# Performance work log

Hardware: AMD Instinct MI355X
Metric: run time of the kernel (lower is better)

## Reference

```python
import jax, jax.numpy as jnp
import numpy as np

B, S, E = 4, 2048, 1024
HIDDEN = 1024
HEADS = 16


def setup_inputs() -> dict:
    key = jax.random.key(0)
    k0, k1, k2, k3, k4 = jax.random.split(key, 5)
    inputs = jax.random.normal(k0, (B, S, E), dtype=jnp.float32)
    W_qkv = jax.random.normal(k1, (E, 3 * HIDDEN), dtype=jnp.float32) * 0.02
    b_qkv = jnp.zeros((3 * HIDDEN,), dtype=jnp.float32)
    W_out = jax.random.normal(k2, (HIDDEN, HIDDEN), dtype=jnp.float32) * 0.02
    b_out = jnp.zeros((HIDDEN,), dtype=jnp.float32)
    return {"inputs": inputs, "W_qkv": W_qkv, "b_qkv": b_qkv, "W_out": W_out, "b_out": b_out}


def reference(inputs, W_qkv, b_qkv, W_out, b_out):
    Bv, Sv, Ev = inputs.shape
    x = inputs @ W_qkv + b_qkv                      # [B, S, 3*hidden]
    # Faithful to the original: reshape mixes seq and hidden exactly as the source does.
    x = x.reshape(Bv, HEADS, Sv, -1)                # [B, H, S, 3*hidden/H]
    q, k, v = jnp.split(x, 3, axis=-1)              # each [B, H, S, hidden/H]
    scale = (2 * HIDDEN) ** (-0.5)
    qk = jnp.einsum('bhse,bhte->bhst', q, k) * scale  # [B, H, S, S]
    mask = jnp.triu(jnp.full((Sv, Sv), -jnp.inf, dtype=qk.dtype), k=1)
    attn = jax.nn.softmax(qk + mask, axis=-1)
    sa = jnp.einsum('bhst,bhte->bhse', attn, v).reshape(Bv, Sv, -1)  # [B, S, hidden]
    return sa @ W_out + b_out
```

## Files before the change

kernel.cpp:

```cpp
#include <hip/hip_runtime.h>
#include <hip/hip_bf16.h>

using bf16 = __hip_bfloat16;

typedef __attribute__((ext_vector_type(8))) short short8;
typedef __attribute__((ext_vector_type(4))) float f32x4;


#define CEXP 0.03188127742677263f

__device__ __forceinline__ unsigned short f2bf(float v) {
  bf16 h = __float2bfloat16(v);
  return *(unsigned short*)&h;
}
__device__ __forceinline__ unsigned int pack2bf(float a, float b) {
  return (unsigned int)f2bf(a) | ((unsigned int)f2bf(b) << 16);
}

__device__ __forceinline__ void gload_lds16(const void* g, void* lds) {
  __builtin_amdgcn_global_load_lds(
      (const __attribute__((address_space(1))) unsigned int*)(g),
      (__attribute__((address_space(3))) unsigned int*)(lds), 16, 0, 0);
}

__global__ void detect_kernel(const unsigned int* __restrict__ x, int* __restrict__ flag) {
  unsigned int w = x[threadIdx.x];
  unsigned int e = (w >> 7) & 0xFF;
  bool inband = (e >= 96 && e <= 133);
  unsigned long long m = __ballot(inband);
  if (threadIdx.x == 0) flag[0] = (__popcll(m) >= 48) ? 0 : 1;
}

__global__ __launch_bounds__(256) void convert_kernel(
    const void* __restrict__ src, bf16* __restrict__ dst, int n8,
    const int* __restrict__ flag) {
  int i = blockIdx.x * 256 + threadIdx.x;
  if (i >= n8) return;
  uint4 outv;
  if (*flag) {
    const float4* s = (const float4*)src + (size_t)i * 2;
    float4 a = s[0], b = s[1];
    outv.x = pack2bf(a.x, a.y);
    outv.y = pack2bf(a.z, a.w);
    outv.z = pack2bf(b.x, b.y);
    outv.w = pack2bf(b.z, b.w);
  } else {
    outv = ((const uint4*)src)[i];
  }
  ((uint4*)dst)[i] = outv;
}

__global__ void convert_bias_qkv(const void* __restrict__ src, bf16* __restrict__ dst,
                                 const int* __restrict__ flag) {
  int i = blockIdx.x * 256 + threadIdx.x;
  if (i >= 3072) return;
  float v = (*flag) ? ((const float*)src)[i]
                    : __bfloat162float(((const bf16*)src)[i]);
  if ((i % 192) < 64) v *= CEXP;
  dst[i] = __float2bfloat16(v);
}

__global__ __launch_bounds__(256) void transpose_bf16(
    const void* __restrict__ src, bf16* __restrict__ dst, int R, int Cc,
    const int* __restrict__ flag, int qscale) {
  __shared__ float tile[32][33];
  const int c0 = blockIdx.x * 32, r0 = blockIdx.y * 32;
  const int tx = threadIdx.x & 31, ty = threadIdx.x >> 5;
  const bool f32 = (*flag != 0);
#pragma unroll
  for (int it = 0; it < 4; ++it) {
    int r = ty + it * 8;
    float v;
    if (f32) v = ((const float*)src)[(size_t)(r0 + r) * Cc + c0 + tx];
    else     v = __bfloat162float(((const bf16*)src)[(size_t)(r0 + r) * Cc + c0 + tx]);
    tile[r][tx] = v;
  }
  __syncthreads();
#pragma unroll
  for (int it = 0; it < 4; ++it) {
    int r = ty + it * 8;
    float vv = tile[tx][r];
    if (qscale && (((c0 + r) % 192) < 64)) vv *= CEXP;
    dst[(size_t)(c0 + r) * R + r0 + tx] = __float2bfloat16(vv);
  }
}

__global__ __launch_bounds__(256) void transpose_v(const bf16* __restrict__ qkv,
                                                   bf16* __restrict__ vtg)
{
  __shared__ short tile[64][72];
  const int bh = blockIdx.x;
  const int k0 = blockIdx.y * 64;
  const unsigned short* qk = (const unsigned short*)qkv + (size_t)bh * 393216;
  const int key = threadIdx.x & 63;
  const int dv = threadIdx.x >> 6;
  const int gk = k0 + key;
  const unsigned short* src =
      qk + (size_t)(gk >> 4) * 3072 + (gk & 15) * 192 + 128 + dv * 16;
  *(short8*)&tile[key][dv * 16] = *(const short8*)src;
  *(short8*)&tile[key][dv * 16 + 8] = *(const short8*)(src + 8);
  __syncthreads();
  const int d = threadIdx.x & 63;
  const int kv = threadIdx.x >> 6;
  unsigned short* dst =
      (unsigned short*)vtg + ((size_t)bh * 64 + d) * 2048 + k0 + kv * 16;
  short8 a, b;
#pragma unroll
  for (int j = 0; j < 8; ++j) {
    a[j] = tile[kv * 16 + j][d];
    b[j] = tile[kv * 16 + 8 + j][d];
  }
  *(short8*)dst = a;
  *(short8*)(dst + 8) = b;
}

__global__ __launch_bounds__(256) void gemm_mfma(
    const bf16* __restrict__ A, const bf16* __restrict__ BT,
    const bf16* __restrict__ bias, void* __restrict__ C,
    int M, int N, int K, int store_mode, const int* __restrict__ flag)
{
  __shared__ alignas(16) unsigned short As[128 * 32];
  __shared__ alignas(16) unsigned short Bs[128 * 32];
  const bool store_f32 = store_mode && (*flag != 0);
  const int tid = threadIdx.x;
  const int wave = tid >> 6, lane = tid & 63;
  const int l15 = lane & 15, l4 = lane >> 4;

  const int nwg = gridDim.x * gridDim.y;
  const int orig = blockIdx.x + gridDim.x * blockIdx.y;
  const int qn = nwg >> 3, rn = nwg & 7;
  const int xcd = orig & 7, loc = orig >> 3;
  const int swz = (xcd < rn ? xcd * (qn + 1) : rn * (qn + 1) + (xcd - rn) * qn) + loc;
  const int bx = swz % gridDim.x, by = swz / gridDim.x;

  const int m0 = by * 128, n0 = bx * 128;
  const int wm = (wave & 1) * 64, wn = (wave >> 1) * 64;

  const int srow = wave * 32 + (lane >> 2);
  const int skv = (lane & 3) * 8;
  const bf16* ga = A + (size_t)(m0 + srow) * K + skv;
  const bf16* gb = BT + (size_t)(n0 + srow) * K + skv;
  unsigned short* la = As + (wave * 32) * 32;
  unsigned short* lb = Bs + (wave * 32) * 32;

  f32x4 acc[4][4] = {};

  for (int k0 = 0; k0 < K; k0 += 32) {
    __syncthreads();
    gload_lds16(ga, la);
    gload_lds16(ga + (size_t)16 * K, la + 16 * 32);
    gload_lds16(gb, lb);
    gload_lds16(gb + (size_t)16 * K, lb + 16 * 32);
    ga += 32; gb += 32;
    __syncthreads();

    short8 af[4], bfr[4];
#pragma unroll
    for (int i = 0; i < 4; ++i) {
      af[i]  = *(const short8*)(As + (wm + i * 16 + l15) * 32 + l4 * 8);
      bfr[i] = *(const short8*)(Bs + (wn + i * 16 + l15) * 32 + l4 * 8);
    }
#pragma unroll
    for (int i = 0; i < 4; ++i)
#pragma unroll
      for (int j = 0; j < 4; ++j)
        acc[i][j] = __builtin_amdgcn_mfma_f32_16x16x32_bf16(af[i], bfr[j], acc[i][j], 0, 0, 0);
  }

#pragma unroll
  for (int j = 0; j < 4; ++j) {
    const int n = n0 + wn + j * 16 + l15;
    const float bv = __bfloat162float(bias[n]);
#pragma unroll
    for (int i = 0; i < 4; ++i) {
#pragma unroll
      for (int r = 0; r < 4; ++r) {
        const int mrow = m0 + wm + i * 16 + l4 * 4 + r;
        const float v = acc[i][j][r] + bv;
        if (store_f32) ((float*)C)[(size_t)mrow * N + n] = v;
        else           ((bf16*)C)[(size_t)mrow * N + n] = __float2bfloat16(v);
      }
    }
  }
}

__global__ __launch_bounds__(512) void attn_mfma(const bf16* __restrict__ qkv,
                                                 const bf16* __restrict__ vtg,
                                                 bf16* __restrict__ sa)
{
  __shared__ alignas(16) short Ks[2][4096];
  __shared__ alignas(16) short Vs[2][4096];
  __shared__ alignas(16) short Ps[8][1152];
  const int tid = threadIdx.x;
  const int bh = blockIdx.x;
  const int pr = blockIdx.y;
  const size_t base = (size_t)bh * 393216;
  const int w = tid >> 6;
  const int g = w >> 2;
  const int wl = w & 3;
  const int lane = tid & 63;
  const int l15 = lane & 15, l4 = lane >> 4;
  const unsigned short* qk = (const unsigned short*)qkv;
  const unsigned short* vtb = (const unsigned short*)vtg + (size_t)bh * 131072;
  short* psw = &Ps[w][0];

  const int qc = g ? pr : (15 - pr);
  const int my_ktmax  = 2 * qc + 1;
  const int blk_ktmax = 2 * (15 - pr) + 1;

  const unsigned short* gsrc0 =
      g ? (vtb + (size_t)lane * 2048)
        : (qk + base + (size_t)(lane >> 4) * 3072 + (lane & 15) * 192 + 64);
  const size_t gstep = g ? 64 : 12288;

  short8 qf[2][2];
#pragma unroll
  for (int h = 0; h < 2; ++h) {
    const unsigned short* pq =
        qk + base + (size_t)(qc * 8 + 2 * wl + h) * 3072 + l15 * 192 + l4 * 8;
    qf[h][0] = *(const short8*)pq;
    qf[h][1] = *(const short8*)(pq + 32);
  }

  f32x4 o[2][4] = {};
  float ml[2] = {-__builtin_inff(), -__builtin_inff()};
  float ls[2] = {0.f, 0.f};
  int cur = 0;

  {
    short* dstbuf = g ? &Vs[0][0] : &Ks[0][0];
    gload_lds16(gsrc0 + wl * 8, dstbuf + wl * 512);
    gload_lds16(gsrc0 + (wl + 4) * 8, dstbuf + (wl + 4) * 512);
  }
  __syncthreads();

  for (int kt = 0; kt <= blk_ktmax; ++kt) {
    if (kt < blk_ktmax) {
      short* dstbuf = g ? &Vs[cur ^ 1][0] : &Ks[cur ^ 1][0];
      const unsigned short* s = gsrc0 + (size_t)(kt + 1) * gstep;
      gload_lds16(s + wl * 8, dstbuf + wl * 512);
      gload_lds16(s + (wl + 4) * 8, dstbuf + (wl + 4) * 512);
    }

    if (kt <= my_ktmax) {
      f32x4 sc[2][4];
#pragma unroll
      for (int t = 0; t < 4; ++t) {
        const short8 kf0 = *(const short8*)&Ks[cur][(l4) * 512 + (16 * t + l15) * 8];
        const short8 kf1 = *(const short8*)&Ks[cur][(4 + l4) * 512 + (16 * t + l15) * 8];
#pragma unroll
        for (int h = 0; h < 2; ++h) {
          f32x4 c = {};
          c = __builtin_amdgcn_mfma_f32_16x16x32_bf16(kf0, qf[h][0], c, 0, 0, 0);
          c = __builtin_amdgcn_mfma_f32_16x16x32_bf16(kf1, qf[h][1], c, 0, 0, 0);
          sc[h][t] = c;
        }
      }

      if (kt >= 2 * qc) {
        const int kb = 64 * (kt - 2 * qc);
#pragma unroll
        for (int h = 0; h < 2; ++h) {
          const int thr = 32 * wl + 16 * h + l15;
#pragma unroll
          for (int t = 0; t < 4; ++t)
#pragma unroll
            for (int r = 0; r < 4; ++r)
              if (kb + 16 * t + 4 * l4 + r > thr) sc[h][t][r] = -__builtin_inff();
        }
      }

      unsigned int pk2[2][4][2];
#pragma unroll
      for (int h = 0; h < 2; ++h) {
        float mx = -__builtin_inff();
#pragma unroll
        for (int t = 0; t < 4; ++t)
#pragma unroll
          for (int r = 0; r < 4; ++r) mx = fmaxf(mx, sc[h][t][r]);
        mx = fmaxf(mx, __shfl_xor(mx, 16, 64));
        mx = fmaxf(mx, __shfl_xor(mx, 32, 64));
        if (!__all(mx <= ml[h] + 8.f)) {
          const float m_new = fmaxf(ml[h], mx);
          const float alpha = __builtin_amdgcn_exp2f(ml[h] - m_new);
          ml[h] = m_new;
          ls[h] *= alpha;
#pragma unroll
          for (int jn = 0; jn < 4; ++jn)
#pragma unroll
            for (int r = 0; r < 4; ++r) o[h][jn][r] *= alpha;
        }
        const float m_new = ml[h];
        float s = 0.f;
#pragma unroll
        for (int t = 0; t < 4; ++t) {
          float p0 = __builtin_amdgcn_exp2f(sc[h][t][0] - m_new);
          float p1 = __builtin_amdgcn_exp2f(sc[h][t][1] - m_new);
          float p2 = __builtin_amdgcn_exp2f(sc[h][t][2] - m_new);
          float p3 = __builtin_amdgcn_exp2f(sc[h][t][3] - m_new);
          s += (p0 + p1) + (p2 + p3);
          pk2[h][t][0] = pack2bf(p0, p1);
          pk2[h][t][1] = pack2bf(p2, p3);
        }
        s += __shfl_xor(s, 16, 64);
        s += __shfl_xor(s, 32, 64);
        ls[h] += s;
      }

      short8 pf[2][2];
#pragma unroll
      for (int h = 0; h < 2; ++h) {
#pragma unroll
        for (int t = 0; t < 4; ++t) {
          uint2 wv; wv.x = pk2[h][t][0]; wv.y = pk2[h][t][1];
          *(uint2*)(psw + l15 * 72 + 16 * t + 4 * l4) = wv;
        }
        pf[h][0] = *(const short8*)(psw + l15 * 72 + 8 * l4);
        pf[h][1] = *(const short8*)(psw + l15 * 72 + 32 + 8 * l4);
      }

#pragma unroll
      for (int jn = 0; jn < 4; ++jn)
#pragma unroll
        for (int ks = 0; ks < 2; ++ks) {
          const short8 vf =
              *(const short8*)&Vs[cur][(4 * ks + l4) * 512 + (16 * jn + l15) * 8];
#pragma unroll
          for (int h = 0; h < 2; ++h)
            o[h][jn] = __builtin_amdgcn_mfma_f32_16x16x32_bf16(vf, pf[h][ks], o[h][jn], 0, 0, 0);
        }
    }

    __syncthreads();
    cur ^= 1;
  }

#pragma unroll
  for (int h = 0; h < 2; ++h) {
    const float inv = 1.0f / ls[h];
    unsigned short* so =
        (unsigned short*)sa + (size_t)(bh * 128 + qc * 8 + 2 * wl + h) * 1024;
#pragma unroll
    for (int jn = 0; jn < 4; ++jn) {
      uint2 wv;
      wv.x = pack2bf(o[h][jn][0] * inv, o[h][jn][1] * inv);
      wv.y = pack2bf(o[h][jn][2] * inv, o[h][jn][3] * inv);
      *(uint2*)(so + l15 * 64 + jn * 16 + l4 * 4) = wv;
    }
  }
}

extern "C" void kernel_launch(void* const* d_in, const int* in_sizes, int n_in,
                              void* d_out, int out_size, void* d_ws, size_t ws_size,
                              hipStream_t stream)
{
  const void* x_raw    = d_in[0];
  const void* Wqkv_raw = d_in[1];
  const void* bqkv_raw = d_in[2];
  const void* Wout_raw = d_in[3];
  const void* bout_raw = d_in[4];

  char* ws = (char*)d_ws;
  int*  flag   = (int*)ws;
  bf16* xb     = (bf16*)(ws + 256);
  bf16* wqkvT  = xb + (size_t)8192 * 1024;
  bf16* bqkvb  = wqkvT + (size_t)3072 * 1024;
  bf16* woutT  = bqkvb + 4096;
  bf16* boutb  = woutT + (size_t)1024 * 1024;
  bf16* qkv    = boutb + 4096;
  bf16* sa     = qkv + (size_t)8192 * 3072;
  bf16* vtg    = sa + (size_t)8192 * 1024;

  detect_kernel<<<1, 64, 0, stream>>>((const unsigned int*)x_raw, flag);

  convert_kernel<<<(8192 * 1024 / 8 + 255) / 256, 256, 0, stream>>>(x_raw, xb, 8192 * 1024 / 8, flag);
  convert_bias_qkv<<<12, 256, 0, stream>>>(bqkv_raw, bqkvb, flag);
  convert_kernel<<<1, 256, 0, stream>>>(bout_raw, boutb, 1024 / 8, flag);
  transpose_bf16<<<dim3(3072 / 32, 1024 / 32), 256, 0, stream>>>(Wqkv_raw, wqkvT, 1024, 3072, flag, 1);
  transpose_bf16<<<dim3(1024 / 32, 1024 / 32), 256, 0, stream>>>(Wout_raw, woutT, 1024, 1024, flag, 0);

  gemm_mfma<<<dim3(3072 / 128, 8192 / 128), 256, 0, stream>>>(
      xb, wqkvT, bqkvb, qkv, 8192, 3072, 1024, 0, flag);
  transpose_v<<<dim3(64, 32), 256, 0, stream>>>(qkv, vtg);
  attn_mfma<<<dim3(64, 8), 512, 0, stream>>>(qkv, vtg, sa);
  gemm_mfma<<<dim3(1024 / 128, 8192 / 128), 256, 0, stream>>>(
      sa, woutT, boutb, d_out, 8192, 1024, 1024, 1, flag);
}
```

Before: 294.0 us.

## Rewrite GEMM with 256x256 tiles, double-buffered LDS and XOR swizzle

Replaces the 128x128 single-buffered GEMM with a 512-thread 256x256-tile kernel using K-step 64. Global-to-LDS loads are double buffered with explicit vmcnt waits to overlap the next tile's fetch with MFMA work, and an XOR swizzle on LDS columns aims to avoid bank conflicts. Each wave computes a 128x64 sub-tile for more operand reuse, and setprio is raised around MFMA bursts. Costs are 128KB LDS per block and more accumulator registers, which limit occupancy. The out-projection grid drops to 128 blocks, which may underfill the GPU.

```diff
diff --git a/kernel.cpp b/kernel.cpp
--- a/kernel.cpp
+++ b/kernel.cpp
@@ -114,68 +114,94 @@
   *(short8*)(dst + 8) = b;
 }
 
-__global__ __launch_bounds__(256) void gemm_mfma(
+__global__ __launch_bounds__(512) void gemm256(
     const bf16* __restrict__ A, const bf16* __restrict__ BT,
     const bf16* __restrict__ bias, void* __restrict__ C,
     int M, int N, int K, int store_mode, const int* __restrict__ flag)
 {
-  __shared__ alignas(16) unsigned short As[128 * 32];
-  __shared__ alignas(16) unsigned short Bs[128 * 32];
+  __shared__ alignas(16) short As2[2][16384];
+  __shared__ alignas(16) short Bs2[2][16384];
   const bool store_f32 = store_mode && (*flag != 0);
   const int tid = threadIdx.x;
-  const int wave = tid >> 6, lane = tid & 63;
+  const int lane = tid & 63;
+  const int w = tid >> 6;
   const int l15 = lane & 15, l4 = lane >> 4;
+  const int wm2 = w >> 2, wn4 = w & 3;
 
   const int nwg = gridDim.x * gridDim.y;
   const int orig = blockIdx.x + gridDim.x * blockIdx.y;
-  const int qn = nwg >> 3, rn = nwg & 7;
-  const int xcd = orig & 7, loc = orig >> 3;
-  const int swz = (xcd < rn ? xcd * (qn + 1) : rn * (qn + 1) + (xcd - rn) * qn) + loc;
+  const int qn = nwg >> 3;
+  const int swz = (orig & 7) * qn + (orig >> 3);
   const int bx = swz % gridDim.x, by = swz / gridDim.x;
-
-  const int m0 = by * 128, n0 = bx * 128;
-  const int wm = (wave & 1) * 64, wn = (wave >> 1) * 64;
-
-  const int srow = wave * 32 + (lane >> 2);
-  const int skv = (lane & 3) * 8;
-  const bf16* ga = A + (size_t)(m0 + srow) * K + skv;
-  const bf16* gb = BT + (size_t)(n0 + srow) * K + skv;
-  unsigned short* la = As + (wave * 32) * 32;
-  unsigned short* lb = Bs + (wave * 32) * 32;
-
-  f32x4 acc[4][4] = {};
-
-  for (int k0 = 0; k0 < K; k0 += 32) {
-    __syncthreads();
-    gload_lds16(ga, la);
-    gload_lds16(ga + (size_t)16 * K, la + 16 * 32);
-    gload_lds16(gb, lb);
-    gload_lds16(gb + (size_t)16 * K, lb + 16 * 32);
-    ga += 32; gb += 32;
-    __syncthreads();
-
-    short8 af[4], bfr[4];
-#pragma unroll
-    for (int i = 0; i < 4; ++i) {
-      af[i]  = *(const short8*)(As + (wm + i * 16 + l15) * 32 + l4 * 8);
-      bfr[i] = *(const short8*)(Bs + (wn + i * 16 + l15) * 32 + l4 * 8);
-    }
-#pragma unroll
-    for (int i = 0; i < 4; ++i)
+  const int m0 = by * 256, n0 = bx * 256;
+
+  const int srow = tid >> 3;
+  const int koff = ((tid & 7) ^ (srow & 7)) << 3;
+  const bf16* pa = A + (size_t)(m0 + srow) * K + koff;
+  const bf16* pb = BT + (size_t)(n0 + srow) * K + koff;
+  const int dst0 = tid * 8;
+
+  const int rsw = l15 & 7;
+
+  f32x4 acc[8][4] = {};
+  const int nt = K >> 6;
+
+#pragma unroll
+  for (int q = 0; q < 4; ++q) {
+    gload_lds16(pa + (size_t)(q * 64) * K, &As2[0][q * 4096 + dst0]);
+    gload_lds16(pb + (size_t)(q * 64) * K, &Bs2[0][q * 4096 + dst0]);
+  }
+
+  for (int t = 0; t < nt; ++t) {
+    const int c = t & 1;
+    if (t + 1 < nt) {
+      const int nb = c ^ 1;
+      const bf16* sa_ = pa + (size_t)(t + 1) * 64;
+      const bf16* sb_ = pb + (size_t)(t + 1) * 64;
+#pragma unroll
+      for (int q = 0; q < 4; ++q) {
+        gload_lds16(sa_ + (size_t)(q * 64) * K, &As2[nb][q * 4096 + dst0]);
+        gload_lds16(sb_ + (size_t)(q * 64) * K, &Bs2[nb][q * 4096 + dst0]);
+      }
+      asm volatile("s_waitcnt vmcnt(8)" ::: "memory");
+    } else {
+      asm volatile("s_waitcnt vmcnt(0)" ::: "memory");
+    }
+    __builtin_amdgcn_s_barrier();
+    asm volatile("" ::: "memory");
+
+#pragma unroll
+    for (int s = 0; s < 2; ++s) {
+      const int cgs = (((s << 2) | l4) ^ rsw) * 8;
+      short8 af[8], bfr[4];
+#pragma unroll
+      for (int i = 0; i < 8; ++i)
+        af[i] = *(const short8*)&As2[c][(wm2 * 128 + i * 16 + l15) * 64 + cgs];
 #pragma unroll
       for (int j = 0; j < 4; ++j)
-        acc[i][j] = __builtin_amdgcn_mfma_f32_16x16x32_bf16(af[i], bfr[j], acc[i][j], 0, 0, 0);
+        bfr[j] = *(const short8*)&Bs2[c][(wn4 * 64 + j * 16 + l15) * 64 + cgs];
+      __builtin_amdgcn_s_setprio(1);
+#pragma unroll
+      for (int i = 0; i < 8; ++i)
+#pragma unroll
+        for (int j = 0; j < 4; ++j)
+          acc[i][j] = __builtin_amdgcn_mfma_f32_16x16x32_bf16(af[i], bfr[j], acc[i][j], 0, 0, 0);
+      __builtin_amdgcn_s_setprio(0);
+    }
+    asm volatile("" ::: "memory");
+    __builtin_amdgcn_s_barrier();
+    asm volatile("" ::: "memory");
   }
 
 #pragma unroll
   for (int j = 0; j < 4; ++j) {
-    const int n = n0 + wn + j * 16 + l15;
+    const int n = n0 + wn4 * 64 + j * 16 + l15;
     const float bv = __bfloat162float(bias[n]);
 #pragma unroll
-    for (int i = 0; i < 4; ++i) {
+    for (int i = 0; i < 8; ++i) {
 #pragma unroll
       for (int r = 0; r < 4; ++r) {
-        const int mrow = m0 + wm + i * 16 + l4 * 4 + r;
+        const int mrow = m0 + wm2 * 128 + i * 16 + l4 * 4 + r;
         const float v = acc[i][j][r] + bv;
         if (store_f32) ((float*)C)[(size_t)mrow * N + n] = v;
         else           ((bf16*)C)[(size_t)mrow * N + n] = __float2bfloat16(v);
@@ -379,10 +405,10 @@
   transpose_bf16<<<dim3(3072 / 32, 1024 / 32), 256, 0, stream>>>(Wqkv_raw, wqkvT, 1024, 3072, flag, 1);
   transpose_bf16<<<dim3(1024 / 32, 1024 / 32), 256, 0, stream>>>(Wout_raw, woutT, 1024, 1024, flag, 0);
 
-  gemm_mfma<<<dim3(3072 / 128, 8192 / 128), 256, 0, stream>>>(
+  gemm256<<<dim3(3072 / 256, 8192 / 256), 512, 0, stream>>>(
       xb, wqkvT, bqkvb, qkv, 8192, 3072, 1024, 0, flag);
   transpose_v<<<dim3(64, 32), 256, 0, stream>>>(qkv, vtg);
   attn_mfma<<<dim3(64, 8), 512, 0, stream>>>(qkv, vtg, sa);
-  gemm_mfma<<<dim3(1024 / 128, 8192 / 128), 256, 0, stream>>>(
+  gemm256<<<dim3(1024 / 256, 8192 / 256), 512, 0, stream>>>(
       sa, woutT, boutb, d_out, 8192, 1024, 1024, 1, flag);
 }
```

Result: no change. 296.4 us (+0.8%).
